# Performance work log

Measured on AMD Instinct MI355X. Metric: run time of the kernel, lower is better.

## Reference

```python
import jax, jax.numpy as jnp
import numpy as np

N_NODES = 100000
N_EDGES = 1000000
D = 64
OUT = 64
EPS = 1e-5


def setup_inputs() -> dict:
    key = jax.random.key(0)
    k1, k2, k3, k4 = jax.random.split(key, 4)
    x = jax.random.normal(k1, (N_NODES, D), dtype=jnp.float32)
    edge_index = jax.random.randint(k2, (2, N_EDGES), 0, N_NODES, dtype=jnp.int64)
    # Linear(2*D, OUT): torch default init ~ U(-1/sqrt(fan_in), 1/sqrt(fan_in))
    bound = 1.0 / np.sqrt(2 * D)
    W = jax.random.uniform(k3, (2 * D, OUT), minval=-bound, maxval=bound, dtype=jnp.float32)
    b = jax.random.uniform(k4, (OUT,), minval=-bound, maxval=bound, dtype=jnp.float32)
    gamma = jnp.ones((OUT,), dtype=jnp.float32)
    beta = jnp.zeros((OUT,), dtype=jnp.float32)
    return {"x": x, "edge_index": edge_index, "W": W, "b": b, "gamma": gamma, "beta": beta}


def reference(x, edge_index, W, b, gamma, beta):
    row, col = edge_index[0], edge_index[1]
    # gather source features and scatter-add into destination nodes
    neighbor_sum = jax.ops.segment_sum(x[row], col, num_segments=x.shape[0])  # [N, D]
    h = jnp.concatenate([x, neighbor_sum], axis=-1)  # [N, 2D]
    h = h @ W + b  # [N, OUT]
    # LayerNorm over last dim
    mu = jnp.mean(h, axis=-1, keepdims=True)
    var = jnp.var(h, axis=-1, keepdims=True)
    h = (h - mu) * jax.lax.rsqrt(var + EPS) * gamma + beta
    return h
```

## Files before the change

### kernel.cpp

```cpp
#include <hip/hip_runtime.h>

#define NN 100000
#define NE 1000000
#define OUT_D 64
#define EPS 1e-5f

#define NB 196
#define COLS 512
#define BSTRIDE 6016
#define PBSTRIDE 8064
#define EPB 4096
#define NBLK1 245
#define NPROJ 1024

#define NOUTB 2048

#define WSTRIDE 136

typedef __attribute__((ext_vector_type(8))) short bf16x8;
typedef __attribute__((ext_vector_type(4))) float f32x4;
typedef __attribute__((ext_vector_type(4))) int i32x4;

static __device__ __forceinline__ unsigned short f2bf(float f) {
    unsigned u = __float_as_uint(f);
    u += 0x7FFFu + ((u >> 16) & 1u);
    return (unsigned short)(u >> 16);
}
static __device__ __forceinline__ float bf2f(unsigned short s) {
    return __uint_as_float((unsigned)s << 16);
}

__global__ __launch_bounds__(256) void mega_kernel(
    const float* __restrict__ x, const float* __restrict__ W,
    const int* __restrict__ ei, int* __restrict__ gcur, unsigned* __restrict__ gbuf,
    unsigned short* __restrict__ y1, unsigned short* __restrict__ y2)
{
    __shared__ __align__(16) char smem[23648];
    const int tid = threadIdx.x;
    const int lane = tid & 63;
    const int wv = tid >> 6;

    if (blockIdx.x < NBLK1) {
        int*           lcnt  = (int*)smem;
        int*           loff  = (int*)(smem + 784);
        int*           lbase = (int*)(smem + 1572);
        int*           lcur  = (int*)(smem + 2356);
        int*           wpart = (int*)(smem + 3140);
        unsigned*      lbuf  = (unsigned*)(smem + 3156);
        unsigned char* lbkt  = (unsigned char*)(smem + 19540);
        const int e0 = blockIdx.x * EPB;

        int rows[16], cols[16];
        #pragma unroll
        for (int j = 0; j < 16; ++j) {
            const int e = e0 + j * 256 + tid;
            const bool v = e < NE;
            rows[j] = v ? ei[e] : 0;
            cols[j] = v ? ei[NE + e] : -1;
        }
        for (int i = tid; i < NB; i += 256) lcnt[i] = 0;
        __syncthreads();
        #pragma unroll
        for (int j = 0; j < 16; ++j)
            if (cols[j] >= 0) atomicAdd(&lcnt[cols[j] >> 9], 1);
        __syncthreads();
        {
            const int c = (tid < NB) ? lcnt[tid] : 0;
            int s = c;
            #pragma unroll
            for (int o = 1; o < 64; o <<= 1) { int t = __shfl_up(s, o); if (lane >= o) s += t; }
            if (lane == 63) wpart[wv] = s;
            __syncthreads();
            int woff = 0;
            for (int ww = 0; ww < wv; ++ww) woff += wpart[ww];
            if (tid < NB) {
                loff[tid] = woff + s - c;
                lcur[tid] = woff + s - c;
                lbase[tid] = atomicAdd(&gcur[tid], c);
            }
            if (tid == NB - 1) loff[NB] = woff + s;
        }
        __syncthreads();
        #pragma unroll
        for (int j = 0; j < 16; ++j) {
            if (cols[j] >= 0) {
                const int b = cols[j] >> 9;
                const int p = atomicAdd(&lcur[b], 1);
                lbuf[p] = ((unsigned)rows[j] << 9) | (unsigned)(cols[j] & (COLS - 1));
                lbkt[p] = (unsigned char)b;
            }
        }
        __syncthreads();
        const int total = loff[NB];
        for (int t = tid; t < total; t += 256) {
            const int b = lbkt[t];
            const unsigned idx = (unsigned)(lbase[b] + (t - loff[b]));
            if (idx < BSTRIDE) gbuf[(size_t)b * BSTRIDE + idx] = lbuf[t];
        }
    } else {
        if (blockIdx.x == NBLK1 && tid < OUT_D)
            y2[(size_t)NN * OUT_D + tid] = 0;
        unsigned short* wlds = (unsigned short*)smem;
        for (int i = tid; i < 128 * 64; i += 256) {
            const int krow = i >> 6, col = i & 63;
            wlds[col * WSTRIDE + krow] = f2bf(W[i]);
        }
        __syncthreads();
        const int m = lane & 15;
        const int quad = lane >> 4;
        bf16x8 Wf[8][2];
        #pragma unroll
        for (int t = 0; t < 8; ++t)
            #pragma unroll
            for (int q = 0; q < 2; ++q) {
                const int krow0 = q * 32 + quad * 8 + ((t < 4) ? 0 : 64);
                const int col = (t & 3) * 16 + m;
                Wf[t][q] = *(const bf16x8*)(wlds + col * WSTRIDE + krow0);
            }
        for (int tile = (blockIdx.x - NBLK1) * 4 + wv; tile < NN / 16; tile += NPROJ * 4) {
            const int n0 = tile * 16;
            bf16x8 Af[2];
            #pragma unroll
            for (int q = 0; q < 2; ++q) {
                const float* px = x + (size_t)(n0 + m) * 64 + q * 32 + quad * 8;
                const f32x4 a0 = *(const f32x4*)px;
                const f32x4 a1 = *(const f32x4*)(px + 4);
                bf16x8 f;
                #pragma unroll
                for (int j = 0; j < 4; ++j) { f[j] = (short)f2bf(a0[j]); f[4 + j] = (short)f2bf(a1[j]); }
                Af[q] = f;
            }
            #pragma unroll
            for (int t = 0; t < 8; ++t) {
                f32x4 acc = {0.f, 0.f, 0.f, 0.f};
                acc = __builtin_amdgcn_mfma_f32_16x16x32_bf16(Af[0], Wf[t][0], acc, 0, 0, 0);
                acc = __builtin_amdgcn_mfma_f32_16x16x32_bf16(Af[1], Wf[t][1], acc, 0, 0, 0);
                unsigned short* __restrict__ dst = (t < 4) ? y1 : y2;
                const int colb = (t & 3) * 16 + m;
                #pragma unroll
                for (int r = 0; r < 4; ++r)
                    dst[(size_t)(n0 + quad * 4 + r) * 64 + colb] = f2bf(acc[r]);
            }
        }
    }
}

__global__ __launch_bounds__(512) void place_kernel(
    const int* __restrict__ gcur, const unsigned* __restrict__ gbuf,
    int* __restrict__ csr, unsigned* __restrict__ rowpack)
{
    __shared__ int cofs[COLS + 1];
    __shared__ int ccur[COLS];
    __shared__ unsigned lsrc[BSTRIDE];
    __shared__ int ldst[PBSTRIDE];
    const int b = blockIdx.x, tid = threadIdx.x;
    const int n0 = b << 9;

    for (int i = tid; i < COLS; i += 512) cofs[i] = 0;
    for (int i = tid; i < PBSTRIDE; i += 512) ldst[i] = NN;
    __syncthreads();
    const int cntE = min(gcur[b], BSTRIDE);
    const unsigned* __restrict__ gb = gbuf + (size_t)b * BSTRIDE;

    for (int i = tid; i < cntE; i += 512) {
        const unsigned p = gb[i];
        lsrc[i] = p;
        atomicAdd(&cofs[p & (COLS - 1)], 1);
    }
    __syncthreads();
    if (tid < 64) {
        int v[8], tsum = 0;
        #pragma unroll
        for (int k = 0; k < 8; ++k) { v[k] = (cofs[tid * 8 + k] + 3) & ~3; tsum += v[k]; }
        int s = tsum;
        #pragma unroll
        for (int o = 1; o < 64; o <<= 1) { int t = __shfl_up(s, o); if (tid >= o) s += t; }
        int run = s - tsum;
        #pragma unroll
        for (int k = 0; k < 8; ++k) { cofs[tid * 8 + k] = run; ccur[tid * 8 + k] = run; run += v[k]; }
        if (tid == 63) cofs[COLS] = run;
    }
    __syncthreads();
    for (int i = tid; i < cntE; i += 512) {
        const unsigned p = lsrc[i];
        const int pos = atomicAdd(&ccur[p & (COLS - 1)], 1);
        ldst[pos] = (int)(p >> 9);
    }
    __syncthreads();
    const int ptotal = cofs[COLS];
    const int base = b * PBSTRIDE;
    for (int i = tid; i < ptotal; i += 512) csr[base + i] = ldst[i];
    const int ncols = min(COLS, NN - n0);
    for (int c = tid; c < ncols; c += 512) {
        const int st = cofs[c];
        const int len = min(cofs[c + 1] - st, 511);
        rowpack[n0 + c] = ((unsigned)st << 9) | (unsigned)len;
    }
}

__global__ __launch_bounds__(256) void out_kernel(
    const unsigned* __restrict__ rowpack, const int* __restrict__ csr,
    const unsigned short* __restrict__ y1, const unsigned short* __restrict__ y2,
    const float* __restrict__ bias, const float* __restrict__ gamma,
    const float* __restrict__ beta, float* __restrict__ out)
{
    const int lane = threadIdx.x & 63;
    const int wid0 = __builtin_amdgcn_readfirstlane(blockIdx.x * 4 + (threadIdx.x >> 6));
    const float bi = bias[lane], ga = gamma[lane], be = beta[lane];

    for (int n = wid0; n < NN; n += NOUTB * 4) {
        const unsigned pk = rowpack[n];
        const int cnt = (int)(pk & 511);
        const i32x4* __restrict__ cs =
            (const i32x4*)(csr + (n >> 9) * PBSTRIDE + (int)(pk >> 9));

        float acc = bf2f(y1[(size_t)n * OUT_D + lane]) + bi;
        int i = 0;
        for (; i + 8 <= cnt; i += 8) {
            const i32x4 c0 = cs[(i >> 2)];
            const i32x4 c1 = cs[(i >> 2) + 1];
            const float v0 = bf2f(y2[(size_t)c0[0] * OUT_D + lane]);
            const float v1 = bf2f(y2[(size_t)c0[1] * OUT_D + lane]);
            const float v2 = bf2f(y2[(size_t)c0[2] * OUT_D + lane]);
            const float v3 = bf2f(y2[(size_t)c0[3] * OUT_D + lane]);
            const float v4 = bf2f(y2[(size_t)c1[0] * OUT_D + lane]);
            const float v5 = bf2f(y2[(size_t)c1[1] * OUT_D + lane]);
            const float v6 = bf2f(y2[(size_t)c1[2] * OUT_D + lane]);
            const float v7 = bf2f(y2[(size_t)c1[3] * OUT_D + lane]);
            acc += ((v0 + v1) + (v2 + v3)) + ((v4 + v5) + (v6 + v7));
        }
        if (i < cnt) {
            const i32x4 c0 = cs[(i >> 2)];
            const float v0 = bf2f(y2[(size_t)c0[0] * OUT_D + lane]);
            const float v1 = bf2f(y2[(size_t)c0[1] * OUT_D + lane]);
            const float v2 = bf2f(y2[(size_t)c0[2] * OUT_D + lane]);
            const float v3 = bf2f(y2[(size_t)c0[3] * OUT_D + lane]);
            acc += (v0 + v1) + (v2 + v3);
        }

        float sv = acc, sq = acc * acc;
        #pragma unroll
        for (int off = 32; off; off >>= 1) { sv += __shfl_xor(sv, off); sq += __shfl_xor(sq, off); }
        const float mu  = sv * (1.0f / OUT_D);
        const float var = sq * (1.0f / OUT_D) - mu * mu;
        const float inv = rsqrtf(var + EPS);
        out[(size_t)n * OUT_D + lane] = (acc - mu) * inv * ga + be;
    }
}

extern "C" void kernel_launch(void* const* d_in, const int* in_sizes, int n_in,
                              void* d_out, int out_size, void* d_ws, size_t ws_size,
                              hipStream_t stream) {
    const float* x     = (const float*)d_in[0];
    const int*   ei    = (const int*)  d_in[1];
    const float* W     = (const float*)d_in[2];
    const float* b     = (const float*)d_in[3];
    const float* gamma = (const float*)d_in[4];
    const float* beta  = (const float*)d_in[5];
    float* out = (float*)d_out;

    char* p = (char*)d_ws;
    int*            gcur    = (int*)p;             p += 1024;
    unsigned*       gbuf    = (unsigned*)p;        p += (size_t)NB * BSTRIDE * 4;
    int*            csr     = (int*)p;             p += (size_t)NB * PBSTRIDE * 4;
    unsigned*       rowpack = (unsigned*)p;        p += (size_t)(NB * COLS) * 4;
    unsigned short* y1      = (unsigned short*)p;  p += (size_t)NN * OUT_D * 2;
    unsigned short* y2      = (unsigned short*)p;

    hipMemsetAsync(gcur, 0, NB * sizeof(int), stream);
    mega_kernel <<<NBLK1 + NPROJ, 256, 0, stream>>>(x, W, ei, gcur, gbuf, y1, y2);
    place_kernel<<<NB, 512, 0, stream>>>(gcur, gbuf, csr, rowpack);
    out_kernel  <<<NOUTB, 256, 0, stream>>>(rowpack, csr, y1, y2, b, gamma, beta, out);
}
```

Before: 133.3 us.

## Process two nodes per wavefront with packed bf16x2 gathers and prefetched rowpack

```diff
diff --git a/kernel.cpp b/kernel.cpp
--- a/kernel.cpp
+++ b/kernel.cpp
@@ -14,6 +14,7 @@
 #define NPROJ 1024
 
 #define NOUTB 2048
+#define NITER 7
 
 #define WSTRIDE 136
 
@@ -28,6 +29,12 @@
 }
 static __device__ __forceinline__ float bf2f(unsigned short s) {
     return __uint_as_float((unsigned)s << 16);
+}
+static __device__ __forceinline__ float bflo(unsigned g) {
+    return __uint_as_float(g << 16);
+}
+static __device__ __forceinline__ float bfhi(unsigned g) {
+    return __uint_as_float(g & 0xffff0000u);
 }
 
 __global__ __launch_bounds__(256) void mega_kernel(
@@ -204,47 +211,78 @@
     const float* __restrict__ bias, const float* __restrict__ gamma,
     const float* __restrict__ beta, float* __restrict__ out)
 {
-    const int lane = threadIdx.x & 63;
-    const int wid0 = __builtin_amdgcn_readfirstlane(blockIdx.x * 4 + (threadIdx.x >> 6));
-    const float bi = bias[lane], ga = gamma[lane], be = beta[lane];
-
-    for (int n = wid0; n < NN; n += NOUTB * 4) {
-        const unsigned pk = rowpack[n];
+    const int tid = threadIdx.x;
+    const int lane = tid & 63;
+    const int half = lane >> 5;
+    const int sl = lane & 31;
+    const int nb = blockIdx.x * 8 + ((tid >> 6) << 1) + half;
+    const unsigned* __restrict__ y2u = (const unsigned*)y2;
+    const unsigned* __restrict__ y1u = (const unsigned*)y1;
+
+    const float bi0 = bias[2 * sl],  bi1 = bias[2 * sl + 1];
+    const float ga0 = gamma[2 * sl], ga1 = gamma[2 * sl + 1];
+    const float be0 = beta[2 * sl],  be1 = beta[2 * sl + 1];
+
+    unsigned pks[NITER];
+    #pragma unroll
+    for (int it = 0; it < NITER; ++it) {
+        const int n = it * (NOUTB * 8) + nb;
+        pks[it] = (n < NN) ? rowpack[n] : 0u;
+    }
+
+    #pragma unroll
+    for (int it = 0; it < NITER; ++it) {
+        const int n = it * (NOUTB * 8) + nb;
+        if (n >= NN) continue;
+        const unsigned pk = pks[it];
         const int cnt = (int)(pk & 511);
         const i32x4* __restrict__ cs =
             (const i32x4*)(csr + (n >> 9) * PBSTRIDE + (int)(pk >> 9));
 
-        float acc = bf2f(y1[(size_t)n * OUT_D + lane]) + bi;
+        const unsigned gy = y1u[(size_t)n * 32 + sl];
+        float a0 = bflo(gy) + bi0;
+        float a1 = bfhi(gy) + bi1;
+
         int i = 0;
         for (; i + 8 <= cnt; i += 8) {
             const i32x4 c0 = cs[(i >> 2)];
             const i32x4 c1 = cs[(i >> 2) + 1];
-            const float v0 = bf2f(y2[(size_t)c0[0] * OUT_D + lane]);
-            const float v1 = bf2f(y2[(size_t)c0[1] * OUT_D + lane]);
-            const float v2 = bf2f(y2[(size_t)c0[2] * OUT_D + lane]);
-            const float v3 = bf2f(y2[(size_t)c0[3] * OUT_D + lane]);
-            const float v4 = bf2f(y2[(size_t)c1[0] * OUT_D + lane]);
-            const float v5 = bf2f(y2[(size_t)c1[1] * OUT_D + lane]);
-            const float v6 = bf2f(y2[(size_t)c1[2] * OUT_D + lane]);
-            const float v7 = bf2f(y2[(size_t)c1[3] * OUT_D + lane]);
-            acc += ((v0 + v1) + (v2 + v3)) + ((v4 + v5) + (v6 + v7));
+            const unsigned g0 = y2u[(size_t)c0[0] * 32 + sl];
+            const unsigned g1 = y2u[(size_t)c0[1] * 32 + sl];
+            const unsigned g2 = y2u[(size_t)c0[2] * 32 + sl];
+            const unsigned g3 = y2u[(size_t)c0[3] * 32 + sl];
+            const unsigned g4 = y2u[(size_t)c1[0] * 32 + sl];
+            const unsigned g5 = y2u[(size_t)c1[1] * 32 + sl];
+            const unsigned g6 = y2u[(size_t)c1[2] * 32 + sl];
+            const unsigned g7 = y2u[(size_t)c1[3] * 32 + sl];
+            a0 += ((bflo(g0) + bflo(g1)) + (bflo(g2) + bflo(g3))) +
+                  ((bflo(g4) + bflo(g5)) + (bflo(g6) + bflo(g7)));
+            a1 += ((bfhi(g0) + bfhi(g1)) + (bfhi(g2) + bfhi(g3))) +
+                  ((bfhi(g4) + bfhi(g5)) + (bfhi(g6) + bfhi(g7)));
         }
         if (i < cnt) {
             const i32x4 c0 = cs[(i >> 2)];
-            const float v0 = bf2f(y2[(size_t)c0[0] * OUT_D + lane]);
-            const float v1 = bf2f(y2[(size_t)c0[1] * OUT_D + lane]);
-            const float v2 = bf2f(y2[(size_t)c0[2] * OUT_D + lane]);
-            const float v3 = bf2f(y2[(size_t)c0[3] * OUT_D + lane]);
-            acc += (v0 + v1) + (v2 + v3);
-        }
-
-        float sv = acc, sq = acc * acc;
-        #pragma unroll
-        for (int off = 32; off; off >>= 1) { sv += __shfl_xor(sv, off); sq += __shfl_xor(sq, off); }
+            const unsigned g0 = y2u[(size_t)c0[0] * 32 + sl];
+            const unsigned g1 = y2u[(size_t)c0[1] * 32 + sl];
+            const unsigned g2 = y2u[(size_t)c0[2] * 32 + sl];
+            const unsigned g3 = y2u[(size_t)c0[3] * 32 + sl];
+            a0 += (bflo(g0) + bflo(g1)) + (bflo(g2) + bflo(g3));
+            a1 += (bfhi(g0) + bfhi(g1)) + (bfhi(g2) + bfhi(g3));
+        }
+
+        float sv = a0 + a1, sq = a0 * a0 + a1 * a1;
+        #pragma unroll
+        for (int off = 16; off; off >>= 1) {
+            sv += __shfl_xor(sv, off);
+            sq += __shfl_xor(sq, off);
+        }
         const float mu  = sv * (1.0f / OUT_D);
         const float var = sq * (1.0f / OUT_D) - mu * mu;
         const float inv = rsqrtf(var + EPS);
-        out[(size_t)n * OUT_D + lane] = (acc - mu) * inv * ga + be;
+        float2 o;
+        o.x = (a0 - mu) * inv * ga0 + be0;
+        o.y = (a1 - mu) * inv * ga1 + be1;
+        *(float2*)(out + (size_t)n * OUT_D + 2 * sl) = o;
     }
 }
 
```

Result: slower. 142.3 us (+6.7%).
